# Kernel tuning notes

Measured on AMD Instinct MI355X. Metric: run time of the kernel, lower is better.

## Reference

```python
import jax, jax.numpy as jnp
import numpy as np

NUM_FEATURE = 512
HIDDEN = 256
NUM_CLASSES = 10
L1 = 1e-4
ALPHA = 1e-3
BATCH = 65536


def setup_inputs() -> dict:
    key = jax.random.key(0)
    k = jax.random.split(key, 6)
    x = jax.random.normal(k[0], (BATCH, NUM_FEATURE), dtype=jnp.float32)
    y = jax.random.randint(k[1], (BATCH,), 0, NUM_CLASSES, dtype=jnp.int32)
    fc0 = jax.random.normal(k[2], (NUM_FEATURE, 512), dtype=jnp.float32) / NUM_FEATURE
    fc1 = jax.random.normal(k[3], (NUM_FEATURE, 512), dtype=jnp.float32) / NUM_FEATURE
    w = jax.random.normal(k[4], (NUM_FEATURE, HIDDEN), dtype=jnp.float32) / NUM_FEATURE
    w1 = jax.random.normal(k[5], (HIDDEN, NUM_CLASSES), dtype=jnp.float32) / HIDDEN
    return {"x": x, "y": y, "fc0": fc0, "fc1": fc1, "w": w, "w1": w1}


def reference(x, y, fc0, fc1, w, w1):
    # sigmoid-gated MLP block with residual
    x1 = x @ fc0                                   # [B, 512]
    x2 = jax.nn.relu(x @ fc1)                      # [B, 512]
    x4 = x + (1.0 + jax.nn.sigmoid(x1)) * x2       # [B, 512] residual

    # head (Dropout(p=0.0) is identity)
    logits = jax.nn.relu(x4 @ w) @ w1              # [B, 10]
    pred = jnp.argmax(logits, axis=1)

    # cross-entropy (mean over batch)
    logp = jax.nn.log_softmax(logits, axis=-1)
    ce = -jnp.mean(jnp.take_along_axis(logp, y[:, None].astype(jnp.int32), axis=1))

    # L1 penalty on all weight matrices
    l1_pen = L1 * (jnp.abs(w1).sum() + jnp.abs(w).sum()
                   + jnp.abs(fc0).sum() + jnp.abs(fc1).sum())

    # per-class variance: sum_i ||mean_{y_i} - x4_i||^2, vectorized via segment sums
    counts = jax.ops.segment_sum(jnp.ones((x4.shape[0],), jnp.float32), y,
                                 num_segments=NUM_CLASSES)
    sums = jax.ops.segment_sum(x4, y, num_segments=NUM_CLASSES)   # [10, 512]
    means = sums / jnp.maximum(counts, 1.0)[:, None]
    var_loss = jnp.sum(jnp.square(means[y] - x4))

    loss = ce + l1_pen + ALPHA * var_loss
    acc = jnp.mean((pred.astype(jnp.int32) == y.astype(jnp.int32)).astype(jnp.float32))
    return (loss, acc)
```

## Files before the change

kernel.cpp:

```cpp
#include <hip/hip_runtime.h>
#include <stdint.h>

#define BATCH 65536
#define FDIM 512
#define HDIM 256
#define NC 10
#define NREP 16

typedef short short8 __attribute__((ext_vector_type(8)));
typedef float f32x4 __attribute__((ext_vector_type(4)));

#define OFF_FC0T   ((size_t)0)
#define OFF_FC1T   (OFF_FC0T + (size_t)512*512*2)
#define OFF_WT     (OFF_FC1T + (size_t)512*512*2)
#define OFF_XT     (OFF_WT   + (size_t)256*512*2)
#define OFF_X4T    (OFF_XT   + (size_t)BATCH*512*2)
#define OFF_ACC    (OFF_X4T  + (size_t)BATCH*512*2)
#define SCAL_SUMSQ 0
#define SCAL_CE    16
#define SCAL_ACC   32
#define SCAL_L1    48
#define SCAL_N     128
#define CNT_OFF    SCAL_N
#define GSUM_OFF   (SCAL_N + NREP*16)
#define ACC_FLOATS (GSUM_OFF + NREP*5120)
#define OFF_W1T    (OFF_ACC + (size_t)ACC_FLOATS*4)

#define GLL(g,l) __builtin_amdgcn_global_load_lds((const __attribute__((address_space(1))) void*)(g), (__attribute__((address_space(3))) void*)(l), 16, 0, 0)

__device__ __forceinline__ unsigned short f2b(float f){
  unsigned u = __float_as_uint(f);
  u += 0x7FFFu + ((u >> 16) & 1u);
  return (unsigned short)(u >> 16);
}
__device__ __forceinline__ float b2f(unsigned short h){
  return __uint_as_float(((unsigned)h) << 16);
}
__device__ __forceinline__ unsigned pk2b(float f0, float f1){
  unsigned u0 = __float_as_uint(f0) + 0x8000u;
  unsigned u1 = __float_as_uint(f1) + 0x8000u;
  return __builtin_amdgcn_perm(u1, u0, 0x07060302u);
}

__global__ __launch_bounds__(256) void k_setup(
    const float* __restrict__ x,   const float* __restrict__ fc0,
    const float* __restrict__ fc1, const float* __restrict__ w,
    const float* __restrict__ w1,
    unsigned short* __restrict__ xT,   unsigned short* __restrict__ fc0T,
    unsigned short* __restrict__ fc1T, unsigned short* __restrict__ wT,
    unsigned short* __restrict__ w1T,  float* __restrict__ accb)
{
  int blk = blockIdx.x, t = threadIdx.x;
  if (blk < 1024){
    int I = blk*4 + (t >> 6);
    int l = t & 63;
    int row = I*16 + (l & 15), q = l >> 4;
    const float* src = x + (size_t)row*FDIM + q*8;
    #pragma unroll
    for (int C = 0; C < 16; ++C){
      float4 v0 = *(const float4*)(src + C*32);
      float4 v1 = *(const float4*)(src + C*32 + 4);
      unsigned o[4];
      o[0] = pk2b(v0.x, v0.y); o[1] = pk2b(v0.z, v0.w);
      o[2] = pk2b(v1.x, v1.y); o[3] = pk2b(v1.z, v1.w);
      *(short8*)&xT[(((size_t)I*16 + C) << 9) + l*8] = *(short8*)o;
    }
    return;
  }
  if (blk < 1360){
    int i = (blk - 1024)*256 + t;
    float l1v = 0.f;
    if (i < 32768){
      int n4 = i&15, m = (i>>4)&3, C = (i>>6)&15, J = i>>10;
      int n = J*16+n4, k8 = C*4+m;
      unsigned short o[8];
      #pragma unroll
      for (int j=0;j<8;++j){ float v = fc0[(size_t)(k8*8+j)*512 + n]; o[j]=f2b(v); l1v += fabsf(v); }
      *(short8*)&fc0T[(size_t)(J*16+C)*512 + (i&63)*8] = *(short8*)o;
    } else if (i < 65536){
      int j0 = i - 32768;
      int n4 = j0&15, m = (j0>>4)&3, C = (j0>>6)&15, J = j0>>10;
      int n = J*16+n4, k8 = C*4+m;
      unsigned short o[8];
      #pragma unroll
      for (int j=0;j<8;++j){ float v = fc1[(size_t)(k8*8+j)*512 + n]; o[j]=f2b(v); l1v += fabsf(v); }
      *(short8*)&fc1T[(size_t)(J*16+C)*512 + (j0&63)*8] = *(short8*)o;
    } else if (i < 81920){
      int j0 = i - 65536;
      int n4 = j0&15, m = (j0>>4)&3, C = (j0>>6)&15, J = j0>>10;
      int n = J*16+n4, k8 = C*4+m;
      unsigned short o[8];
      #pragma unroll
      for (int j=0;j<8;++j){ float v = w[(size_t)(k8*8+j)*256 + n]; o[j]=f2b(v); l1v += fabsf(v); }
      *(short8*)&wT[(size_t)(J*16+C)*512 + (j0&63)*8] = *(short8*)o;
    } else if (i < 86016){
      int j0 = i - 81920;
      int C = j0 >> 9, l = (j0 >> 3) & 63, e = j0 & 7;
      int n = l & 15, k = C*32 + (l>>4)*8 + e;
      float v = (n < NC) ? w1[k*NC + n] : 0.f;
      w1T[C*512 + l*8 + e] = f2b(v);
      if (n < NC) l1v = fabsf(v);
    }
    for (int off = 32; off; off >>= 1) l1v += __shfl_down(l1v, off);
    if ((t & 63) == 0 && l1v != 0.f)
      atomicAdd(&accb[SCAL_L1 + (blk & (NREP-1))], l1v);
    return;
  }
  {
    int base = (blk - 1360)*1024;
    #pragma unroll
    for (int j=0;j<4;++j){
      int idx = base + j*256 + t;
      if (idx < ACC_FLOATS) accb[idx] = 0.f;
    }
  }
}

__global__ __launch_bounds__(256) void k_gemm12(
    const unsigned short* __restrict__ xT,
    const unsigned short* __restrict__ fc0T,
    const unsigned short* __restrict__ fc1T,
    unsigned short* __restrict__ x4T,
    float* __restrict__ scal)
{
  __shared__ __align__(16) char lds[32768];
  unsigned short* As    = (unsigned short*)lds;
  unsigned short* Bs0   = (unsigned short*)(lds + 16384);
  unsigned short* Bs1   = (unsigned short*)(lds + 24576);
  unsigned short* trans = (unsigned short*)(lds + 16384);
  __shared__ float red[4];

  int blk = blockIdx.x;
  int xcd = blk & 7, s = blk >> 3;
  int rowblk = xcd*64 + (s >> 3);
  int colblk = s & 7;

  int t = threadIdx.x;
  int wv = t >> 6, lane = t & 63, ln = lane & 15, quad = lane >> 4;
  int wr = wv >> 1, wc = wv & 1;

  const f32x4 zv = {0.f,0.f,0.f,0.f};
  f32x4 acc1[4][2], acc2[4][2];
  #pragma unroll
  for (int rt=0;rt<4;++rt){ acc1[rt][0]=zv; acc1[rt][1]=zv; acc2[rt][0]=zv; acc2[rt][1]=zv; }

  const char* xb  = (const char*)xT;
  const char* b0b = (const char*)fc0T;
  const char* b1b = (const char*)fc1T;

  for (int kt = 0; kt < 8; ++kt){
    #pragma unroll
    for (int i = 0; i < 2; ++i)
      #pragma unroll
      for (int c = 0; c < 2; ++c){
        size_t Ig = (size_t)(rowblk*8 + wv*2 + i);
        GLL(xb + ((Ig*16 + kt*2 + c) << 10) + lane*16,
            (char*)As + (((wv*2+i)*2 + c) << 10));
      }
    {
      size_t Jg = (size_t)(colblk*4 + wv);
      const char* g0 = b0b + ((Jg*16 + kt*2) << 10) + lane*16;
      const char* g1 = b1b + ((Jg*16 + kt*2) << 10) + lane*16;
      GLL(g0,        (char*)Bs0 + ((wv*2+0) << 10));
      GLL(g0 + 1024, (char*)Bs0 + ((wv*2+1) << 10));
      GLL(g1,        (char*)Bs1 + ((wv*2+0) << 10));
      GLL(g1 + 1024, (char*)Bs1 + ((wv*2+1) << 10));
    }
    __syncthreads();
    #pragma unroll
    for (int c = 0; c < 2; ++c){
      short8 a[4];
      #pragma unroll
      for (int rt=0;rt<4;++rt)
        a[rt] = *(const short8*)&As[(((wr*4+rt)*2 + c) << 9) + lane*8];
      #pragma unroll
      for (int ct=0;ct<2;++ct){
        int jl = wc*2 + ct;
        short8 b0 = *(const short8*)&Bs0[((jl*2+c) << 9) + lane*8];
        #pragma unroll
        for (int rt=0;rt<4;++rt)
          acc1[rt][ct] = __builtin_amdgcn_mfma_f32_16x16x32_bf16(a[rt], b0, acc1[rt][ct], 0,0,0);
        short8 b1 = *(const short8*)&Bs1[((jl*2+c) << 9) + lane*8];
        #pragma unroll
        for (int rt=0;rt<4;++rt)
          acc2[rt][ct] = __builtin_amdgcn_mfma_f32_16x16x32_bf16(a[rt], b1, acc2[rt][ct], 0,0,0);
      }
    }
    __syncthreads();
  }

  #pragma unroll
  for (int i = 0; i < 2; ++i)
    #pragma unroll
    for (int c = 0; c < 2; ++c){
      size_t Ig = (size_t)(rowblk*8 + wv*2 + i);
      GLL(xb + ((Ig*16 + colblk*2 + c) << 10) + lane*16,
          (char*)As + (((wv*2+i)*2 + c) << 10));
    }
  __syncthreads();

  float sumsq = 0.f;
  #pragma unroll
  for (int rt=0;rt<4;++rt){
    #pragma unroll
    for (int ct=0;ct<2;++ct){
      int slot_hi = (ct*2 + (ln>>3)) << 4;
      int elem = ln & 7;
      #pragma unroll
      for (int r=0;r<4;++r){
        int addr = (((wr*4+rt)*2 + wc) << 9) + ((quad*4+r) | slot_hi)*8 + elem;
        float xv  = b2f(As[addr]);
        float x1v = acc1[rt][ct][r];
        float x2v = fmaxf(acc2[rt][ct][r], 0.f);
        float gate = 1.f + 1.f/(1.f + __expf(-x1v));
        float x4v = fmaf(gate, x2v, xv);
        unsigned short ub = f2b(x4v);
        float fq = b2f(ub);
        sumsq = fmaf(fq, fq, sumsq);
        trans[addr] = ub;
      }
    }
  }
  for (int off = 32; off; off >>= 1) sumsq += __shfl_down(sumsq, off);
  if (lane == 0) red[wv] = sumsq;
  __syncthreads();
  if (t == 0)
    atomicAdd(&scal[SCAL_SUMSQ + (blk & (NREP-1))], red[0]+red[1]+red[2]+red[3]);
  {
    int lt = t >> 4;
    int I_local = lt >> 1, C_local = lt & 1;
    size_t gbase = ((size_t)(rowblk*8 + I_local)*16 + colblk*2 + C_local) << 9;
    int s0 = (t & 15)*32;
    #pragma unroll
    for (int j=0;j<4;++j)
      *(short8*)&x4T[gbase + s0 + j*8] = *(const short8*)&trans[(lt << 9) + s0 + j*8];
  }
}

__global__ __launch_bounds__(256) void k_csum(const unsigned short* __restrict__ x4T,
                                              const int* __restrict__ y,
                                              float* __restrict__ gsum){
  int w = blockIdx.x*4 + (threadIdx.x >> 6);
  int l = threadIdx.x & 63;
  int C = w & 15, Ig = w >> 4;
  int rl = l & 15, q = l >> 4;
  float a[NC][8];
  #pragma unroll
  for (int c=0;c<NC;++c)
    #pragma unroll
    for (int e=0;e<8;++e) a[c][e]=0.f;
  for (int ii = 0; ii < 64; ++ii){
    int I = Ig*64 + ii;
    int yv = y[I*16 + rl];
    short8 v = *(const short8*)&x4T[(((size_t)I*16 + C) << 9) + l*8];
    float f[8];
    #pragma unroll
    for (int e=0;e<8;++e) f[e] = b2f((unsigned short)v[e]);
    #pragma unroll
    for (int c=0;c<NC;++c){
      bool m = (yv == c);
      #pragma unroll
      for (int e=0;e<8;++e) a[c][e] += m ? f[e] : 0.f;
    }
  }
  #pragma unroll
  for (int off = 1; off < 16; off <<= 1)
    #pragma unroll
    for (int c=0;c<NC;++c)
      #pragma unroll
      for (int e=0;e<8;++e) a[c][e] += __shfl_xor(a[c][e], off);
  if (rl == 0){
    int rep = Ig & (NREP-1);
    int kb = C*32 + q*8;
    #pragma unroll
    for (int c=0;c<NC;++c)
      #pragma unroll
      for (int e=0;e<8;++e)
        atomicAdd(&gsum[(size_t)rep*5120 + c*512 + kb + e], a[c][e]);
  }
}

__global__ __launch_bounds__(256) void k_cnt(const int* __restrict__ y,
                                             float* __restrict__ gcnt){
  __shared__ float cntS[NC];
  int t = threadIdx.x;
  if (t < NC) cntS[t] = 0.f;
  __syncthreads();
  int base = blockIdx.x*2048;
  for (int i = t; i < 2048; i += 256) atomicAdd(&cntS[y[base+i]], 1.f);
  __syncthreads();
  if (t < NC) atomicAdd(&gcnt[(blockIdx.x & (NREP-1))*16 + t], cntS[t]);
}

__global__ __launch_bounds__(512) void k_gemm3_head(
    const unsigned short* __restrict__ x4T,
    const unsigned short* __restrict__ wT,
    const unsigned short* __restrict__ w1T,
    const int* __restrict__ y,
    float* __restrict__ scal)
{
  __shared__ __align__(16) char lds[49152];
  unsigned short* As     = (unsigned short*)lds;
  unsigned short* Bs     = (unsigned short*)(lds + 16384);
  unsigned short* transH = (unsigned short*)lds;
  __shared__ __align__(16) unsigned short w1s[4096];
  __shared__ float redc[8], reda[8];

  int blk = blockIdx.x;
  int t = threadIdx.x;
  int wv = t >> 6, lane = t & 63, ln = lane & 15, quad = lane >> 4;
  int wr = wv >> 2, wc = wv & 3;
  int rep = (blk ^ (blk >> 4)) & (NREP-1);

  *(short8*)&w1s[t*8] = *(const short8*)&w1T[t*8];

  const f32x4 zv = {0.f,0.f,0.f,0.f};
  f32x4 acc[4][4];
  #pragma unroll
  for (int rt=0;rt<4;++rt)
    #pragma unroll
    for (int ct=0;ct<4;++ct) acc[rt][ct] = zv;

  const char* ab = (const char*)x4T;
  const char* bb = (const char*)wT;

  for (int kt = 0; kt < 8; ++kt){
    {
      size_t Ig = (size_t)(blk*8 + wv);
      GLL(ab + ((Ig*16 + kt*2 + 0) << 10) + lane*16, (char*)As + ((wv*2+0) << 10));
      GLL(ab + ((Ig*16 + kt*2 + 1) << 10) + lane*16, (char*)As + ((wv*2+1) << 10));
    }
    #pragma unroll
    for (int i = 0; i < 2; ++i)
      #pragma unroll
      for (int c = 0; c < 2; ++c){
        size_t Jg = (size_t)(wv*2 + i);
        GLL(bb + ((Jg*16 + kt*2 + c) << 10) + lane*16,
            (char*)Bs + (((wv*2+i)*2 + c) << 10));
      }
    __syncthreads();
    #pragma unroll
    for (int c = 0; c < 2; ++c){
      short8 a[4];
      #pragma unroll
      for (int rt=0;rt<4;++rt)
        a[rt] = *(const short8*)&As[(((wr*4+rt)*2 + c) << 9) + lane*8];
      #pragma unroll
      for (int ct=0;ct<4;++ct){
        short8 b = *(const short8*)&Bs[(((wc*4+ct)*2 + c) << 9) + lane*8];
        #pragma unroll
        for (int rt=0;rt<4;++rt)
          acc[rt][ct] = __builtin_amdgcn_mfma_f32_16x16x32_bf16(a[rt], b, acc[rt][ct], 0,0,0);
      }
    }
    __syncthreads();
  }

  f32x4 alog = zv;
  #pragma unroll
  for (int hf = 0; hf < 2; ++hf){
    __syncthreads();
    if ((wc >> 1) == hf){
      #pragma unroll
      for (int rt=0;rt<4;++rt)
        #pragma unroll
        for (int ct=0;ct<4;++ct)
          #pragma unroll
          for (int r=0;r<4;++r){
            int row_l = wr*64 + rt*16 + quad*4 + r;
            int ch = (wc & 1)*64 + ct*16 + ln;
            int tile = ((row_l >> 4) << 2) | (ch >> 5);
            int slot = (row_l & 15) | (((ch >> 3) & 3) << 4);
            transH[(tile << 9) + slot*8 + (ch & 7)] = f2b(fmaxf(acc[rt][ct][r], 0.f));
          }
    }
    __syncthreads();
    #pragma unroll
    for (int Cl = 0; Cl < 4; ++Cl){
      short8 a = *(const short8*)&transH[((wv*4 + Cl) << 9) + lane*8];
      short8 b = *(const short8*)&w1s[(hf*4 + Cl)*512 + lane*8];
      alog = __builtin_amdgcn_mfma_f32_16x16x32_bf16(a, b, alog, 0,0,0);
    }
  }

  float ce_l = 0.f, acc_l = 0.f;
  #pragma unroll
  for (int r = 0; r < 4; ++r){
    int grow = blk*128 + wv*16 + quad*4 + r;
    int yv = y[grow];
    float lg = (ln < NC) ? alog[r] : -1e30f;
    float m = lg; int mi = ln;
    #pragma unroll
    for (int mk = 1; mk < 16; mk <<= 1){
      float om = __shfl_xor(m, mk); int oi = __shfl_xor(mi, mk);
      if (om > m || (om == m && oi < mi)){ m = om; mi = oi; }
    }
    float e  = (ln < NC) ? __expf(lg - m) : 0.f;
    float sy = (ln == yv) ? lg : 0.f;
    #pragma unroll
    for (int mk = 1; mk < 16; mk <<= 1){ e += __shfl_xor(e, mk); sy += __shfl_xor(sy, mk); }
    float lse = m + __logf(e);
    if (ln == 0){ ce_l += (lse - sy); acc_l += (mi == yv) ? 1.f : 0.f; }
  }
  ce_l  += __shfl_down(ce_l, 16);  acc_l += __shfl_down(acc_l, 16);
  ce_l  += __shfl_down(ce_l, 32);  acc_l += __shfl_down(acc_l, 32);
  if (lane == 0){ redc[wv] = ce_l; reda[wv] = acc_l; }
  __syncthreads();
  if (t == 0){
    float c = 0.f, a = 0.f;
    #pragma unroll
    for (int i=0;i<8;++i){ c += redc[i]; a += reda[i]; }
    atomicAdd(&scal[SCAL_CE  + rep], c);
    atomicAdd(&scal[SCAL_ACC + rep], a);
  }
}

__global__ __launch_bounds__(1024) void k_final(const float* __restrict__ accb,
                                                float* __restrict__ out){
  const float* gsum = accb + GSUM_OFF;
  const float* gcnt = accb + CNT_OFF;
  int t = threadIdx.x;
  float contrib = 0.f;
  for (int idx = t; idx < 5120; idx += 1024){
    float S = 0.f;
    #pragma unroll
    for (int r = 0; r < NREP; ++r) S += gsum[(size_t)r*5120 + idx];
    int c = idx >> 9;
    float cnt = 0.f;
    #pragma unroll
    for (int r = 0; r < NREP; ++r) cnt += gcnt[r*16 + c];
    contrib += S*S / fmaxf(cnt, 1.f);
  }
  for (int off = 32; off; off >>= 1) contrib += __shfl_down(contrib, off);
  __shared__ float red[16];
  if ((t & 63) == 0) red[t >> 6] = contrib;
  __syncthreads();
  if (t == 0){
    float var2 = 0.f;
    #pragma unroll
    for (int i=0;i<16;++i) var2 += red[i];
    float sumsq=0.f, ce=0.f, acc=0.f, l1=0.f;
    for (int r=0;r<NREP;++r){
      sumsq += accb[SCAL_SUMSQ+r];
      ce    += accb[SCAL_CE+r];
      acc   += accb[SCAL_ACC+r];
      l1    += accb[SCAL_L1+r];
    }
    float var_loss = sumsq - var2;
    out[0] = ce/(float)BATCH + 1e-4f*l1 + 1e-3f*var_loss;
    out[1] = acc/(float)BATCH;
  }
}

extern "C" void kernel_launch(void* const* d_in, const int* in_sizes, int n_in,
                              void* d_out, int out_size, void* d_ws, size_t ws_size,
                              hipStream_t stream){
  (void)in_sizes; (void)n_in; (void)out_size; (void)ws_size;
  const float* x   = (const float*)d_in[0];
  const int*   y   = (const int*)d_in[1];
  const float* fc0 = (const float*)d_in[2];
  const float* fc1 = (const float*)d_in[3];
  const float* w   = (const float*)d_in[4];
  const float* w1  = (const float*)d_in[5];
  char* ws = (char*)d_ws;
  unsigned short* fc0T = (unsigned short*)(ws + OFF_FC0T);
  unsigned short* fc1T = (unsigned short*)(ws + OFF_FC1T);
  unsigned short* wT   = (unsigned short*)(ws + OFF_WT);
  unsigned short* xT   = (unsigned short*)(ws + OFF_XT);
  unsigned short* x4T  = (unsigned short*)(ws + OFF_X4T);
  unsigned short* w1T  = (unsigned short*)(ws + OFF_W1T);
  float* accb = (float*)(ws + OFF_ACC);
  float* scal = accb;
  float* gcnt = accb + CNT_OFF;
  float* gsum = accb + GSUM_OFF;

  k_setup<<<1441, 256, 0, stream>>>(x, fc0, fc1, w, w1, xT, fc0T, fc1T, wT, w1T, accb);
  k_gemm12<<<4096, 256, 0, stream>>>(xT, fc0T, fc1T, x4T, scal);
  k_cnt<<<32, 256, 0, stream>>>(y, gcnt);
  k_csum<<<256, 256, 0, stream>>>(x4T, y, gsum);
  k_gemm3_head<<<512, 512, 0, stream>>>(x4T, wT, w1T, y, scal);
  k_final<<<1, 1024, 0, stream>>>(accb, (float*)d_out);
}
```

Baseline: 409.3 us.

## Widen gemm12 and head tiles per wave, fold class counting into setup

```diff
diff --git a/kernel.cpp b/kernel.cpp
--- a/kernel.cpp
+++ b/kernel.cpp
@@ -19,10 +19,9 @@
 #define SCAL_SUMSQ 0
 #define SCAL_CE    16
 #define SCAL_ACC   32
-#define SCAL_L1    48
-#define SCAL_N     128
-#define CNT_OFF    SCAL_N
-#define GSUM_OFF   (SCAL_N + NREP*16)
+#define CNT_OFF    48
+#define L1P_OFF    304
+#define GSUM_OFF   640
 #define ACC_FLOATS (GSUM_OFF + NREP*5120)
 #define OFF_W1T    (OFF_ACC + (size_t)ACC_FLOATS*4)
 
@@ -45,7 +44,7 @@
 __global__ __launch_bounds__(256) void k_setup(
     const float* __restrict__ x,   const float* __restrict__ fc0,
     const float* __restrict__ fc1, const float* __restrict__ w,
-    const float* __restrict__ w1,
+    const float* __restrict__ w1,  const int* __restrict__ y,
     unsigned short* __restrict__ xT,   unsigned short* __restrict__ fc0T,
     unsigned short* __restrict__ fc1T, unsigned short* __restrict__ wT,
     unsigned short* __restrict__ w1T,  float* __restrict__ accb)
@@ -68,6 +67,7 @@
     return;
   }
   if (blk < 1360){
+    __shared__ float l1red[4];
     int i = (blk - 1024)*256 + t;
     float l1v = 0.f;
     if (i < 32768){
@@ -102,17 +102,28 @@
       if (n < NC) l1v = fabsf(v);
     }
     for (int off = 32; off; off >>= 1) l1v += __shfl_down(l1v, off);
-    if ((t & 63) == 0 && l1v != 0.f)
-      atomicAdd(&accb[SCAL_L1 + (blk & (NREP-1))], l1v);
+    if ((t & 63) == 0) l1red[t >> 6] = l1v;
+    __syncthreads();
+    if (t == 0) accb[L1P_OFF + (blk - 1024)] = l1red[0]+l1red[1]+l1red[2]+l1red[3];
     return;
   }
+  if (blk < 1376){
+    __shared__ float cntS[16];
+    int cb = blk - 1360;
+    if (t < 16) cntS[t] = 0.f;
+    __syncthreads();
+    int base = cb*4096;
+    for (int i = t; i < 4096; i += 256) atomicAdd(&cntS[y[base+i]], 1.f);
+    __syncthreads();
+    if (t < 16) accb[CNT_OFF + cb*16 + t] = cntS[t];
+    return;
+  }
   {
-    int base = (blk - 1360)*1024;
-    #pragma unroll
-    for (int j=0;j<4;++j){
-      int idx = base + j*256 + t;
-      if (idx < ACC_FLOATS) accb[idx] = 0.f;
-    }
+    int zb = blk - 1376;
+    int base = GSUM_OFF + zb*1024;
+    #pragma unroll
+    for (int j=0;j<4;++j) accb[base + j*256 + t] = 0.f;
+    if (zb == 0 && t < 48) accb[t] = 0.f;
   }
 }
 
@@ -123,26 +134,29 @@
     unsigned short* __restrict__ x4T,
     float* __restrict__ scal)
 {
-  __shared__ __align__(16) char lds[32768];
-  unsigned short* As    = (unsigned short*)lds;
-  unsigned short* Bs0   = (unsigned short*)(lds + 16384);
-  unsigned short* Bs1   = (unsigned short*)(lds + 24576);
-  unsigned short* trans = (unsigned short*)(lds + 16384);
+  __shared__ __align__(16) char lds[65536];
+  unsigned short* As   = (unsigned short*)lds;
+  unsigned short* Bs0  = (unsigned short*)(lds + 16384);
+  unsigned short* Bs1  = (unsigned short*)(lds + 32768);
+  unsigned short* Xres = (unsigned short*)lds;
+  unsigned short* trans= (unsigned short*)(lds + 32768);
   __shared__ float red[4];
 
   int blk = blockIdx.x;
   int xcd = blk & 7, s = blk >> 3;
-  int rowblk = xcd*64 + (s >> 3);
-  int colblk = s & 7;
+  int rowblk = xcd*64 + (s >> 2);
+  int colblk = s & 3;
 
   int t = threadIdx.x;
   int wv = t >> 6, lane = t & 63, ln = lane & 15, quad = lane >> 4;
   int wr = wv >> 1, wc = wv & 1;
 
   const f32x4 zv = {0.f,0.f,0.f,0.f};
-  f32x4 acc1[4][2], acc2[4][2];
-  #pragma unroll
-  for (int rt=0;rt<4;++rt){ acc1[rt][0]=zv; acc1[rt][1]=zv; acc2[rt][0]=zv; acc2[rt][1]=zv; }
+  f32x4 acc1[4][4], acc2[4][4];
+  #pragma unroll
+  for (int rt=0;rt<4;++rt)
+    #pragma unroll
+    for (int ct=0;ct<4;++ct){ acc1[rt][ct]=zv; acc2[rt][ct]=zv; }
 
   const char* xb  = (const char*)xT;
   const char* b0b = (const char*)fc0T;
@@ -157,14 +171,15 @@
         GLL(xb + ((Ig*16 + kt*2 + c) << 10) + lane*16,
             (char*)As + (((wv*2+i)*2 + c) << 10));
       }
-    {
-      size_t Jg = (size_t)(colblk*4 + wv);
-      const char* g0 = b0b + ((Jg*16 + kt*2) << 10) + lane*16;
-      const char* g1 = b1b + ((Jg*16 + kt*2) << 10) + lane*16;
-      GLL(g0,        (char*)Bs0 + ((wv*2+0) << 10));
-      GLL(g0 + 1024, (char*)Bs0 + ((wv*2+1) << 10));
-      GLL(g1,        (char*)Bs1 + ((wv*2+0) << 10));
-      GLL(g1 + 1024, (char*)Bs1 + ((wv*2+1) << 10));
+    #pragma unroll
+    for (int m = 0; m < 2; ++m){
+      int J_local = wv + m*4;
+      size_t Jg = (size_t)(colblk*8 + J_local);
+      #pragma unroll
+      for (int c = 0; c < 2; ++c){
+        GLL(b0b + ((Jg*16 + kt*2 + c) << 10) + lane*16, (char*)Bs0 + ((J_local*2 + c) << 10));
+        GLL(b1b + ((Jg*16 + kt*2 + c) << 10) + lane*16, (char*)Bs1 + ((J_local*2 + c) << 10));
+      }
     }
     __syncthreads();
     #pragma unroll
@@ -174,13 +189,13 @@
       for (int rt=0;rt<4;++rt)
         a[rt] = *(const short8*)&As[(((wr*4+rt)*2 + c) << 9) + lane*8];
       #pragma unroll
-      for (int ct=0;ct<2;++ct){
-        int jl = wc*2 + ct;
-        short8 b0 = *(const short8*)&Bs0[((jl*2+c) << 9) + lane*8];
+      for (int ct=0;ct<4;++ct){
+        int jl = wc*4 + ct;
+        short8 b0 = *(const short8*)&Bs0[((jl*2 + c) << 9) + lane*8];
         #pragma unroll
         for (int rt=0;rt<4;++rt)
           acc1[rt][ct] = __builtin_amdgcn_mfma_f32_16x16x32_bf16(a[rt], b0, acc1[rt][ct], 0,0,0);
-        short8 b1 = *(const short8*)&Bs1[((jl*2+c) << 9) + lane*8];
+        short8 b1 = *(const short8*)&Bs1[((jl*2 + c) << 9) + lane*8];
         #pragma unroll
         for (int rt=0;rt<4;++rt)
           acc2[rt][ct] = __builtin_amdgcn_mfma_f32_16x16x32_bf16(a[rt], b1, acc2[rt][ct], 0,0,0);
@@ -190,26 +205,28 @@
   }
 
   #pragma unroll
-  for (int i = 0; i < 2; ++i)
-    #pragma unroll
-    for (int c = 0; c < 2; ++c){
-      size_t Ig = (size_t)(rowblk*8 + wv*2 + i);
-      GLL(xb + ((Ig*16 + colblk*2 + c) << 10) + lane*16,
-          (char*)As + (((wv*2+i)*2 + c) << 10));
-    }
+  for (int i = 0; i < 2; ++i){
+    int I_local = wv*2 + i;
+    size_t Ig = (size_t)(rowblk*8 + I_local);
+    #pragma unroll
+    for (int c = 0; c < 4; ++c)
+      GLL(xb + ((Ig*16 + colblk*4 + c) << 10) + lane*16,
+          (char*)Xres + ((I_local*4 + c) << 10));
+  }
   __syncthreads();
 
   float sumsq = 0.f;
   #pragma unroll
   for (int rt=0;rt<4;++rt){
     #pragma unroll
-    for (int ct=0;ct<2;++ct){
-      int slot_hi = (ct*2 + (ln>>3)) << 4;
+    for (int ct=0;ct<4;++ct){
+      int tile = (wr*4 + rt)*4 + wc*2 + (ct>>1);
+      int slot_hi = ((ct&1)*2 + (ln>>3)) << 4;
       int elem = ln & 7;
       #pragma unroll
       for (int r=0;r<4;++r){
-        int addr = (((wr*4+rt)*2 + wc) << 9) + ((quad*4+r) | slot_hi)*8 + elem;
-        float xv  = b2f(As[addr]);
+        int addr = (tile << 9) + (((quad*4+r) | slot_hi) << 3) + elem;
+        float xv  = b2f(Xres[addr]);
         float x1v = acc1[rt][ct][r];
         float x2v = fmaxf(acc2[rt][ct][r], 0.f);
         float gate = 1.f + 1.f/(1.f + __expf(-x1v));
@@ -227,12 +244,12 @@
   if (t == 0)
     atomicAdd(&scal[SCAL_SUMSQ + (blk & (NREP-1))], red[0]+red[1]+red[2]+red[3]);
   {
-    int lt = t >> 4;
-    int I_local = lt >> 1, C_local = lt & 1;
-    size_t gbase = ((size_t)(rowblk*8 + I_local)*16 + colblk*2 + C_local) << 9;
-    int s0 = (t & 15)*32;
-    #pragma unroll
-    for (int j=0;j<4;++j)
+    int lt = t >> 3;
+    int I_local = lt >> 2, C_local = lt & 3;
+    size_t gbase = ((size_t)(rowblk*8 + I_local)*16 + colblk*4 + C_local) << 9;
+    int s0 = (t & 7)*64;
+    #pragma unroll
+    for (int j=0;j<8;++j)
       *(short8*)&x4T[gbase + s0 + j*8] = *(const short8*)&trans[(lt << 9) + s0 + j*8];
   }
 }
@@ -280,19 +297,7 @@
   }
 }
 
-__global__ __launch_bounds__(256) void k_cnt(const int* __restrict__ y,
-                                             float* __restrict__ gcnt){
-  __shared__ float cntS[NC];
-  int t = threadIdx.x;
-  if (t < NC) cntS[t] = 0.f;
-  __syncthreads();
-  int base = blockIdx.x*2048;
-  for (int i = t; i < 2048; i += 256) atomicAdd(&cntS[y[base+i]], 1.f);
-  __syncthreads();
-  if (t < NC) atomicAdd(&gcnt[(blockIdx.x & (NREP-1))*16 + t], cntS[t]);
-}
-
-__global__ __launch_bounds__(512) void k_gemm3_head(
+__global__ __launch_bounds__(256) void k_gemm3_head(
     const unsigned short* __restrict__ x4T,
     const unsigned short* __restrict__ wT,
     const unsigned short* __restrict__ w1T,
@@ -304,40 +309,44 @@
   unsigned short* Bs     = (unsigned short*)(lds + 16384);
   unsigned short* transH = (unsigned short*)lds;
   __shared__ __align__(16) unsigned short w1s[4096];
-  __shared__ float redc[8], reda[8];
+  __shared__ float redc[4], reda[4];
 
   int blk = blockIdx.x;
   int t = threadIdx.x;
   int wv = t >> 6, lane = t & 63, ln = lane & 15, quad = lane >> 4;
-  int wr = wv >> 2, wc = wv & 3;
+  int wr = wv >> 1, wc = wv & 1;
   int rep = (blk ^ (blk >> 4)) & (NREP-1);
 
-  *(short8*)&w1s[t*8] = *(const short8*)&w1T[t*8];
+  *(short8*)&w1s[t*16]     = *(const short8*)&w1T[t*16];
+  *(short8*)&w1s[t*16 + 8] = *(const short8*)&w1T[t*16 + 8];
 
   const f32x4 zv = {0.f,0.f,0.f,0.f};
-  f32x4 acc[4][4];
+  f32x4 acc[4][8];
   #pragma unroll
   for (int rt=0;rt<4;++rt)
     #pragma unroll
-    for (int ct=0;ct<4;++ct) acc[rt][ct] = zv;
+    for (int ct=0;ct<8;++ct) acc[rt][ct] = zv;
 
   const char* ab = (const char*)x4T;
   const char* bb = (const char*)wT;
 
   for (int kt = 0; kt < 8; ++kt){
-    {
-      size_t Ig = (size_t)(blk*8 + wv);
-      GLL(ab + ((Ig*16 + kt*2 + 0) << 10) + lane*16, (char*)As + ((wv*2+0) << 10));
-      GLL(ab + ((Ig*16 + kt*2 + 1) << 10) + lane*16, (char*)As + ((wv*2+1) << 10));
-    }
     #pragma unroll
     for (int i = 0; i < 2; ++i)
       #pragma unroll
       for (int c = 0; c < 2; ++c){
-        size_t Jg = (size_t)(wv*2 + i);
-        GLL(bb + ((Jg*16 + kt*2 + c) << 10) + lane*16,
-            (char*)Bs + (((wv*2+i)*2 + c) << 10));
-      }
+        size_t Ig = (size_t)(blk*8 + wv*2 + i);
+        GLL(ab + ((Ig*16 + kt*2 + c) << 10) + lane*16,
+            (char*)As + (((wv*2+i)*2 + c) << 10));
+      }
+    #pragma unroll
+    for (int m = 0; m < 4; ++m){
+      int J_local = wv*4 + m;
+      #pragma unroll
+      for (int c = 0; c < 2; ++c)
+        GLL(bb + (((size_t)J_local*16 + kt*2 + c) << 10) + lane*16,
+            (char*)Bs + ((J_local*2 + c) << 10));
+    }
     __syncthreads();
     #pragma unroll
     for (int c = 0; c < 2; ++c){
@@ -346,8 +355,9 @@
       for (int rt=0;rt<4;++rt)
         a[rt] = *(const short8*)&As[(((wr*4+rt)*2 + c) << 9) + lane*8];
       #pragma unroll
-      for (int ct=0;ct<4;++ct){
-        short8 b = *(const short8*)&Bs[(((wc*4+ct)*2 + c) << 9) + lane*8];
+      for (int ct=0;ct<8;++ct){
+        int jl = wc*8 + ct;
+        short8 b = *(const short8*)&Bs[((jl*2 + c) << 9) + lane*8];
         #pragma unroll
         for (int rt=0;rt<4;++rt)
           acc[rt][ct] = __builtin_amdgcn_mfma_f32_16x16x32_bf16(a[rt], b, acc[rt][ct], 0,0,0);
@@ -356,62 +366,66 @@
     __syncthreads();
   }
 
-  f32x4 alog = zv;
+  f32x4 alog[2] = {zv, zv};
   #pragma unroll
   for (int hf = 0; hf < 2; ++hf){
     __syncthreads();
-    if ((wc >> 1) == hf){
+    if (wc == hf){
       #pragma unroll
       for (int rt=0;rt<4;++rt)
         #pragma unroll
-        for (int ct=0;ct<4;++ct)
+        for (int ct=0;ct<8;++ct){
+          int tile = (wr*4 + rt)*4 + (ct>>1);
+          int slot_hi = ((ct&1)*2 + (ln>>3)) << 4;
           #pragma unroll
           for (int r=0;r<4;++r){
-            int row_l = wr*64 + rt*16 + quad*4 + r;
-            int ch = (wc & 1)*64 + ct*16 + ln;
-            int tile = ((row_l >> 4) << 2) | (ch >> 5);
-            int slot = (row_l & 15) | (((ch >> 3) & 3) << 4);
-            transH[(tile << 9) + slot*8 + (ch & 7)] = f2b(fmaxf(acc[rt][ct][r], 0.f));
+            int addr = (tile << 9) + (((quad*4+r) | slot_hi) << 3) + (ln & 7);
+            transH[addr] = f2b(fmaxf(acc[rt][ct][r], 0.f));
           }
-    }
-    __syncthreads();
-    #pragma unroll
-    for (int Cl = 0; Cl < 4; ++Cl){
-      short8 a = *(const short8*)&transH[((wv*4 + Cl) << 9) + lane*8];
-      short8 b = *(const short8*)&w1s[(hf*4 + Cl)*512 + lane*8];
-      alog = __builtin_amdgcn_mfma_f32_16x16x32_bf16(a, b, alog, 0,0,0);
+        }
+    }
+    __syncthreads();
+    #pragma unroll
+    for (int i = 0; i < 2; ++i){
+      int I_h = wv*2 + i;
+      #pragma unroll
+      for (int Cl = 0; Cl < 4; ++Cl){
+        short8 a = *(const short8*)&transH[((I_h*4 + Cl) << 9) + lane*8];
+        short8 b = *(const short8*)&w1s[(hf*4 + Cl)*512 + lane*8];
+        alog[i] = __builtin_amdgcn_mfma_f32_16x16x32_bf16(a, b, alog[i], 0,0,0);
+      }
     }
   }
 
   float ce_l = 0.f, acc_l = 0.f;
   #pragma unroll
-  for (int r = 0; r < 4; ++r){
-    int grow = blk*128 + wv*16 + quad*4 + r;
-    int yv = y[grow];
-    float lg = (ln < NC) ? alog[r] : -1e30f;
-    float m = lg; int mi = ln;
-    #pragma unroll
-    for (int mk = 1; mk < 16; mk <<= 1){
-      float om = __shfl_xor(m, mk); int oi = __shfl_xor(mi, mk);
-      if (om > m || (om == m && oi < mi)){ m = om; mi = oi; }
-    }
-    float e  = (ln < NC) ? __expf(lg - m) : 0.f;
-    float sy = (ln == yv) ? lg : 0.f;
-    #pragma unroll
-    for (int mk = 1; mk < 16; mk <<= 1){ e += __shfl_xor(e, mk); sy += __shfl_xor(sy, mk); }
-    float lse = m + __logf(e);
-    if (ln == 0){ ce_l += (lse - sy); acc_l += (mi == yv) ? 1.f : 0.f; }
+  for (int i = 0; i < 2; ++i){
+    #pragma unroll
+    for (int r = 0; r < 4; ++r){
+      int grow = blk*128 + (wv*2+i)*16 + quad*4 + r;
+      int yv = y[grow];
+      float lg = (ln < NC) ? alog[i][r] : -1e30f;
+      float m = lg; int mi = ln;
+      #pragma unroll
+      for (int mk = 1; mk < 16; mk <<= 1){
+        float om = __shfl_xor(m, mk); int oi = __shfl_xor(mi, mk);
+        if (om > m || (om == m && oi < mi)){ m = om; mi = oi; }
+      }
+      float e  = (ln < NC) ? __expf(lg - m) : 0.f;
+      float sy = (ln == yv) ? lg : 0.f;
+      #pragma unroll
+      for (int mk = 1; mk < 16; mk <<= 1){ e += __shfl_xor(e, mk); sy += __shfl_xor(sy, mk); }
+      float lse = m + __logf(e);
+      if (ln == 0){ ce_l += (lse - sy); acc_l += (mi == yv) ? 1.f : 0.f; }
+    }
   }
   ce_l  += __shfl_down(ce_l, 16);  acc_l += __shfl_down(acc_l, 16);
   ce_l  += __shfl_down(ce_l, 32);  acc_l += __shfl_down(acc_l, 32);
   if (lane == 0){ redc[wv] = ce_l; reda[wv] = acc_l; }
   __syncthreads();
   if (t == 0){
-    float c = 0.f, a = 0.f;
-    #pragma unroll
-    for (int i=0;i<8;++i){ c += redc[i]; a += reda[i]; }
-    atomicAdd(&scal[SCAL_CE  + rep], c);
-    atomicAdd(&scal[SCAL_ACC + rep], a);
+    atomicAdd(&scal[SCAL_CE  + rep], redc[0]+redc[1]+redc[2]+redc[3]);
+    atomicAdd(&scal[SCAL_ACC + rep], reda[0]+reda[1]+reda[2]+reda[3]);
   }
 }
 
@@ -431,20 +445,23 @@
     for (int r = 0; r < NREP; ++r) cnt += gcnt[r*16 + c];
     contrib += S*S / fmaxf(cnt, 1.f);
   }
-  for (int off = 32; off; off >>= 1) contrib += __shfl_down(contrib, off);
-  __shared__ float red[16];
-  if ((t & 63) == 0) red[t >> 6] = contrib;
+  float l1loc = (t < 336) ? accb[L1P_OFF + t] : 0.f;
+  for (int off = 32; off; off >>= 1){
+    contrib += __shfl_down(contrib, off);
+    l1loc   += __shfl_down(l1loc, off);
+  }
+  __shared__ float red[16], redl[16];
+  if ((t & 63) == 0){ red[t >> 6] = contrib; redl[t >> 6] = l1loc; }
   __syncthreads();
   if (t == 0){
-    float var2 = 0.f;
-    #pragma unroll
-    for (int i=0;i<16;++i) var2 += red[i];
-    float sumsq=0.f, ce=0.f, acc=0.f, l1=0.f;
+    float var2 = 0.f, l1 = 0.f;
+    #pragma unroll
+    for (int i=0;i<16;++i){ var2 += red[i]; l1 += redl[i]; }
+    float sumsq=0.f, ce=0.f, acc=0.f;
     for (int r=0;r<NREP;++r){
       sumsq += accb[SCAL_SUMSQ+r];
       ce    += accb[SCAL_CE+r];
       acc   += accb[SCAL_ACC+r];
-      l1    += accb[SCAL_L1+r];
     }
     float var_loss = sumsq - var2;
     out[0] = ce/(float)BATCH + 1e-4f*l1 + 1e-3f*var_loss;
@@ -471,13 +488,11 @@
   unsigned short* w1T  = (unsigned short*)(ws + OFF_W1T);
   float* accb = (float*)(ws + OFF_ACC);
   float* scal = accb;
-  float* gcnt = accb + CNT_OFF;
   float* gsum = accb + GSUM_OFF;
 
-  k_setup<<<1441, 256, 0, stream>>>(x, fc0, fc1, w, w1, xT, fc0T, fc1T, wT, w1T, accb);
-  k_gemm12<<<4096, 256, 0, stream>>>(xT, fc0T, fc1T, x4T, scal);
-  k_cnt<<<32, 256, 0, stream>>>(y, gcnt);
+  k_setup<<<1456, 256, 0, stream>>>(x, fc0, fc1, w, w1, y, xT, fc0T, fc1T, wT, w1T, accb);
+  k_gemm12<<<2048, 256, 0, stream>>>(xT, fc0T, fc1T, x4T, scal);
   k_csum<<<256, 256, 0, stream>>>(x4T, y, gsum);
-  k_gemm3_head<<<512, 512, 0, stream>>>(x4T, wT, w1T, y, scal);
+  k_gemm3_head<<<512, 256, 0, stream>>>(x4T, wT, w1T, y, scal);
   k_final<<<1, 1024, 0, stream>>>(accb, (float*)d_out);
 }
```

Result: slower. 465.4 us (+13.7%).

## Merge class-sum into head GEMM kernel and fold label counts into setup

Applied to the files above, without the earlier changes.

```diff
diff --git a/kernel.cpp b/kernel.cpp
--- a/kernel.cpp
+++ b/kernel.cpp
@@ -19,10 +19,9 @@
 #define SCAL_SUMSQ 0
 #define SCAL_CE    16
 #define SCAL_ACC   32
-#define SCAL_L1    48
-#define SCAL_N     128
-#define CNT_OFF    SCAL_N
-#define GSUM_OFF   (SCAL_N + NREP*16)
+#define CNT_OFF    48
+#define L1P_OFF    304
+#define GSUM_OFF   640
 #define ACC_FLOATS (GSUM_OFF + NREP*5120)
 #define OFF_W1T    (OFF_ACC + (size_t)ACC_FLOATS*4)
 
@@ -45,7 +44,7 @@
 __global__ __launch_bounds__(256) void k_setup(
     const float* __restrict__ x,   const float* __restrict__ fc0,
     const float* __restrict__ fc1, const float* __restrict__ w,
-    const float* __restrict__ w1,
+    const float* __restrict__ w1,  const int* __restrict__ y,
     unsigned short* __restrict__ xT,   unsigned short* __restrict__ fc0T,
     unsigned short* __restrict__ fc1T, unsigned short* __restrict__ wT,
     unsigned short* __restrict__ w1T,  float* __restrict__ accb)
@@ -68,6 +67,7 @@
     return;
   }
   if (blk < 1360){
+    __shared__ float l1red[4];
     int i = (blk - 1024)*256 + t;
     float l1v = 0.f;
     if (i < 32768){
@@ -102,17 +102,28 @@
       if (n < NC) l1v = fabsf(v);
     }
     for (int off = 32; off; off >>= 1) l1v += __shfl_down(l1v, off);
-    if ((t & 63) == 0 && l1v != 0.f)
-      atomicAdd(&accb[SCAL_L1 + (blk & (NREP-1))], l1v);
+    if ((t & 63) == 0) l1red[t >> 6] = l1v;
+    __syncthreads();
+    if (t == 0) accb[L1P_OFF + (blk - 1024)] = l1red[0]+l1red[1]+l1red[2]+l1red[3];
     return;
   }
+  if (blk < 1376){
+    __shared__ float cntS[16];
+    int cb = blk - 1360;
+    if (t < 16) cntS[t] = 0.f;
+    __syncthreads();
+    int base = cb*4096;
+    for (int i = t; i < 4096; i += 256) atomicAdd(&cntS[y[base+i]], 1.f);
+    __syncthreads();
+    if (t < 16) accb[CNT_OFF + cb*16 + t] = cntS[t];
+    return;
+  }
   {
-    int base = (blk - 1360)*1024;
-    #pragma unroll
-    for (int j=0;j<4;++j){
-      int idx = base + j*256 + t;
-      if (idx < ACC_FLOATS) accb[idx] = 0.f;
-    }
+    int zb = blk - 1376;
+    int base = GSUM_OFF + zb*1024;
+    #pragma unroll
+    for (int j=0;j<4;++j) accb[base + j*256 + t] = 0.f;
+    if (zb == 0 && t < 48) accb[t] = 0.f;
   }
 }
 
@@ -237,77 +248,69 @@
   }
 }
 
-__global__ __launch_bounds__(256) void k_csum(const unsigned short* __restrict__ x4T,
-                                              const int* __restrict__ y,
-                                              float* __restrict__ gsum){
-  int w = blockIdx.x*4 + (threadIdx.x >> 6);
-  int l = threadIdx.x & 63;
-  int C = w & 15, Ig = w >> 4;
-  int rl = l & 15, q = l >> 4;
-  float a[NC][8];
-  #pragma unroll
-  for (int c=0;c<NC;++c)
-    #pragma unroll
-    for (int e=0;e<8;++e) a[c][e]=0.f;
-  for (int ii = 0; ii < 64; ++ii){
-    int I = Ig*64 + ii;
-    int yv = y[I*16 + rl];
-    short8 v = *(const short8*)&x4T[(((size_t)I*16 + C) << 9) + l*8];
-    float f[8];
-    #pragma unroll
-    for (int e=0;e<8;++e) f[e] = b2f((unsigned short)v[e]);
-    #pragma unroll
-    for (int c=0;c<NC;++c){
-      bool m = (yv == c);
-      #pragma unroll
-      for (int e=0;e<8;++e) a[c][e] += m ? f[e] : 0.f;
-    }
-  }
-  #pragma unroll
-  for (int off = 1; off < 16; off <<= 1)
-    #pragma unroll
-    for (int c=0;c<NC;++c)
-      #pragma unroll
-      for (int e=0;e<8;++e) a[c][e] += __shfl_xor(a[c][e], off);
-  if (rl == 0){
-    int rep = Ig & (NREP-1);
-    int kb = C*32 + q*8;
-    #pragma unroll
-    for (int c=0;c<NC;++c)
-      #pragma unroll
-      for (int e=0;e<8;++e)
-        atomicAdd(&gsum[(size_t)rep*5120 + c*512 + kb + e], a[c][e]);
-  }
-}
-
-__global__ __launch_bounds__(256) void k_cnt(const int* __restrict__ y,
-                                             float* __restrict__ gcnt){
-  __shared__ float cntS[NC];
-  int t = threadIdx.x;
-  if (t < NC) cntS[t] = 0.f;
-  __syncthreads();
-  int base = blockIdx.x*2048;
-  for (int i = t; i < 2048; i += 256) atomicAdd(&cntS[y[base+i]], 1.f);
-  __syncthreads();
-  if (t < NC) atomicAdd(&gcnt[(blockIdx.x & (NREP-1))*16 + t], cntS[t]);
-}
-
-__global__ __launch_bounds__(512) void k_gemm3_head(
+__global__ __launch_bounds__(512) void k_tail(
     const unsigned short* __restrict__ x4T,
     const unsigned short* __restrict__ wT,
     const unsigned short* __restrict__ w1T,
     const int* __restrict__ y,
-    float* __restrict__ scal)
+    float* __restrict__ scal,
+    float* __restrict__ gsum)
 {
   __shared__ __align__(16) char lds[49152];
+  __shared__ __align__(16) unsigned short w1s[4096];
+  __shared__ float redc[8], reda[8];
+
+  int b = blockIdx.x;
+  int t = threadIdx.x;
+
+  if ((b % 5) == 4){
+    int cb = b / 5;
+    int w = cb*8 + (t >> 6);
+    int l = t & 63;
+    int C = w & 15, Ig = w >> 4;
+    int rl = l & 15, q = l >> 4;
+    float a[NC][8];
+    #pragma unroll
+    for (int c=0;c<NC;++c)
+      #pragma unroll
+      for (int e=0;e<8;++e) a[c][e]=0.f;
+    for (int ii = 0; ii < 64; ++ii){
+      int I = Ig*64 + ii;
+      int yv = y[I*16 + rl];
+      short8 v = *(const short8*)&x4T[(((size_t)I*16 + C) << 9) + l*8];
+      float f[8];
+      #pragma unroll
+      for (int e=0;e<8;++e) f[e] = b2f((unsigned short)v[e]);
+      #pragma unroll
+      for (int c=0;c<NC;++c){
+        bool m = (yv == c);
+        #pragma unroll
+        for (int e=0;e<8;++e) a[c][e] += m ? f[e] : 0.f;
+      }
+    }
+    #pragma unroll
+    for (int off = 1; off < 16; off <<= 1)
+      #pragma unroll
+      for (int c=0;c<NC;++c)
+        #pragma unroll
+        for (int e=0;e<8;++e) a[c][e] += __shfl_xor(a[c][e], off);
+    if (rl == 0){
+      int rep = Ig & (NREP-1);
+      int kb = C*32 + q*8;
+      #pragma unroll
+      for (int c=0;c<NC;++c)
+        #pragma unroll
+        for (int e=0;e<8;++e)
+          atomicAdd(&gsum[(size_t)rep*5120 + c*512 + kb + e], a[c][e]);
+    }
+    return;
+  }
+
+  int blk = (b/5)*4 + (b%5);
   unsigned short* As     = (unsigned short*)lds;
   unsigned short* Bs     = (unsigned short*)(lds + 16384);
   unsigned short* transH = (unsigned short*)lds;
-  __shared__ __align__(16) unsigned short w1s[4096];
-  __shared__ float redc[8], reda[8];
-
-  int blk = blockIdx.x;
-  int t = threadIdx.x;
+
   int wv = t >> 6, lane = t & 63, ln = lane & 15, quad = lane >> 4;
   int wr = wv >> 2, wc = wv & 3;
   int rep = (blk ^ (blk >> 4)) & (NREP-1);
@@ -347,10 +350,10 @@
         a[rt] = *(const short8*)&As[(((wr*4+rt)*2 + c) << 9) + lane*8];
       #pragma unroll
       for (int ct=0;ct<4;++ct){
-        short8 b = *(const short8*)&Bs[(((wc*4+ct)*2 + c) << 9) + lane*8];
+        short8 bfr = *(const short8*)&Bs[(((wc*4+ct)*2 + c) << 9) + lane*8];
         #pragma unroll
         for (int rt=0;rt<4;++rt)
-          acc[rt][ct] = __builtin_amdgcn_mfma_f32_16x16x32_bf16(a[rt], b, acc[rt][ct], 0,0,0);
+          acc[rt][ct] = __builtin_amdgcn_mfma_f32_16x16x32_bf16(a[rt], bfr, acc[rt][ct], 0,0,0);
       }
     }
     __syncthreads();
@@ -378,8 +381,8 @@
     #pragma unroll
     for (int Cl = 0; Cl < 4; ++Cl){
       short8 a = *(const short8*)&transH[((wv*4 + Cl) << 9) + lane*8];
-      short8 b = *(const short8*)&w1s[(hf*4 + Cl)*512 + lane*8];
-      alog = __builtin_amdgcn_mfma_f32_16x16x32_bf16(a, b, alog, 0,0,0);
+      short8 bfr = *(const short8*)&w1s[(hf*4 + Cl)*512 + lane*8];
+      alog = __builtin_amdgcn_mfma_f32_16x16x32_bf16(a, bfr, alog, 0,0,0);
     }
   }
 
@@ -431,20 +434,23 @@
     for (int r = 0; r < NREP; ++r) cnt += gcnt[r*16 + c];
     contrib += S*S / fmaxf(cnt, 1.f);
   }
-  for (int off = 32; off; off >>= 1) contrib += __shfl_down(contrib, off);
-  __shared__ float red[16];
-  if ((t & 63) == 0) red[t >> 6] = contrib;
+  float l1loc = (t < 336) ? accb[L1P_OFF + t] : 0.f;
+  for (int off = 32; off; off >>= 1){
+    contrib += __shfl_down(contrib, off);
+    l1loc   += __shfl_down(l1loc, off);
+  }
+  __shared__ float red[16], redl[16];
+  if ((t & 63) == 0){ red[t >> 6] = contrib; redl[t >> 6] = l1loc; }
   __syncthreads();
   if (t == 0){
-    float var2 = 0.f;
-    #pragma unroll
-    for (int i=0;i<16;++i) var2 += red[i];
-    float sumsq=0.f, ce=0.f, acc=0.f, l1=0.f;
+    float var2 = 0.f, l1 = 0.f;
+    #pragma unroll
+    for (int i=0;i<16;++i){ var2 += red[i]; l1 += redl[i]; }
+    float sumsq=0.f, ce=0.f, acc=0.f;
     for (int r=0;r<NREP;++r){
       sumsq += accb[SCAL_SUMSQ+r];
       ce    += accb[SCAL_CE+r];
       acc   += accb[SCAL_ACC+r];
-      l1    += accb[SCAL_L1+r];
     }
     float var_loss = sumsq - var2;
     out[0] = ce/(float)BATCH + 1e-4f*l1 + 1e-3f*var_loss;
@@ -471,13 +477,10 @@
   unsigned short* w1T  = (unsigned short*)(ws + OFF_W1T);
   float* accb = (float*)(ws + OFF_ACC);
   float* scal = accb;
-  float* gcnt = accb + CNT_OFF;
   float* gsum = accb + GSUM_OFF;
 
-  k_setup<<<1441, 256, 0, stream>>>(x, fc0, fc1, w, w1, xT, fc0T, fc1T, wT, w1T, accb);
+  k_setup<<<1456, 256, 0, stream>>>(x, fc0, fc1, w, w1, y, xT, fc0T, fc1T, wT, w1T, accb);
   k_gemm12<<<4096, 256, 0, stream>>>(xT, fc0T, fc1T, x4T, scal);
-  k_cnt<<<32, 256, 0, stream>>>(y, gcnt);
-  k_csum<<<256, 256, 0, stream>>>(x4T, y, gsum);
-  k_gemm3_head<<<512, 512, 0, stream>>>(x4T, wT, w1T, y, scal);
+  k_tail<<<640, 512, 0, stream>>>(x4T, wT, w1T, y, scal, gsum);
   k_final<<<1, 1024, 0, stream>>>(accb, (float*)d_out);
 }
```

New measurement: 419.5 us. +2.5%, slower.
